# Kernel optimization log

Measured on AMD Instinct MI355X. Metric: run time of the kernel, lower is better.

The kernel has to match this reference:

```python
import jax, jax.numpy as jnp
import numpy as np

DIM = 1024
HEADS = 16
B, N = 4, 2048


def setup_inputs() -> dict:
    key = jax.random.key(0)
    ks = jax.random.split(key, 6)
    scale = DIM ** -0.5
    return {
        "x": jax.random.normal(ks[0], (B, N, DIM), dtype=jnp.float32),
        "mask": jax.random.randint(ks[1], (B, N, N), 0, 2) > 0,
        "Wqkv": jax.random.normal(ks[2], (DIM, 3 * DIM), dtype=jnp.float32) * scale,
        "bqkv": jax.random.normal(ks[3], (3 * DIM,), dtype=jnp.float32) * 0.02,
        "Wproj": jax.random.normal(ks[4], (DIM, DIM), dtype=jnp.float32) * scale,
        "bproj": jax.random.normal(ks[5], (DIM,), dtype=jnp.float32) * 0.02,
    }


def reference(x, mask, Wqkv, bqkv, Wproj, bproj):
    Bs, Ns, C = x.shape
    H = HEADS
    D = C // H
    scale = D ** -0.5
    qkv = x @ Wqkv + bqkv                       # [B, N, 3C]
    qkv = qkv.reshape(Bs, Ns, 3, H, D)          # split (three h d)
    q, k, v = jnp.moveaxis(qkv, 2, 0)           # each [B, N, H, D]
    q = q.transpose(0, 2, 1, 3)                 # [B, H, N, D]
    k = k.transpose(0, 2, 1, 3)
    v = v.transpose(0, 2, 1, 3)
    attn = jnp.einsum("bhnd,bhmd->bhnm", q, k) * scale  # [B, H, N, N]
    attn = jnp.where(mask[:, None, :, :], -jnp.inf, attn)
    attn = jax.nn.softmax(attn, axis=-1)
    out = jnp.einsum("bhnm,bhmd->bhnd", attn, v)        # [B, H, N, D]
    out = out.transpose(0, 2, 1, 3).reshape(Bs, Ns, C)  # [B, N, C]
    return out @ Wproj + bproj
```

## Files before the change

kernel.cpp:

```cpp
#include <hip/hip_runtime.h>
#include <cstdint>
#include <cstddef>

constexpr int kC = 1024;
constexpr int kH = 16;
constexpr int kB = 4;
constexpr int kN = 2048;
constexpr int kD = 64;

#define KQ_SCALE 0.18033688011112042f

typedef unsigned short u16;
typedef unsigned int   u32;
typedef unsigned long long u64;
typedef __bf16 v8bf  __attribute__((ext_vector_type(8)));
typedef __bf16 v4bf  __attribute__((ext_vector_type(4)));
typedef float  v4f   __attribute__((ext_vector_type(4)));
typedef u16    u16x8 __attribute__((ext_vector_type(8)));
typedef u16    u16x4 __attribute__((ext_vector_type(4)));
typedef u32    u32x4 __attribute__((ext_vector_type(4)));

__device__ inline u16 f2bf(float f) {
    union { float f; unsigned u; } v; v.f = f;
    unsigned r = v.u + 0x7FFFu + ((v.u >> 16) & 1u);
    return (u16)(r >> 16);
}

__device__ inline float fast_exp2(float x) {
#if __has_builtin(__builtin_amdgcn_exp2f)
    return __builtin_amdgcn_exp2f(x);
#else
    return __expf(x * 0.6931471805599453f);
#endif
}

__device__ inline void gl2lds16(const u16* g, u16* l) {
    __builtin_amdgcn_global_load_lds(
        (const __attribute__((address_space(1))) void*)g,
        (__attribute__((address_space(3))) void*)l, 16, 0, 0);
}

__global__ __launch_bounds__(256) void cast_bf16_kernel(
    const float* __restrict__ in, u16* __restrict__ outp)
{
    const int i = blockIdx.x * 256 + threadIdx.x;
    const float4 f = ((const float4*)in)[i];
    u16x4 o;
    o.x = f2bf(f.x); o.y = f2bf(f.y); o.z = f2bf(f.z); o.w = f2bf(f.w);
    ((u16x4*)outp)[i] = o;
}

__global__ __launch_bounds__(256) void tpose_cast_kernel(
    const float* __restrict__ W, u16* __restrict__ Wt, int R, int Cc)
{
    __shared__ u16 tile[64][65];
    const int c0 = blockIdx.x * 64;
    const int r0 = blockIdx.y * 64;
    const int t  = threadIdx.x;
#pragma unroll
    for (int it = 0; it < 16; ++it) {
        const int r = it * 4 + (t >> 6);
        const int c = t & 63;
        tile[c][r] = f2bf(W[(size_t)(r0 + r) * Cc + c0 + c]);
    }
    __syncthreads();
#pragma unroll
    for (int it = 0; it < 16; ++it) {
        const int rr = it * 4 + (t >> 6);
        const int cc = t & 63;
        Wt[(size_t)(c0 + rr) * R + r0 + cc] = tile[rr][cc];
    }
}

__global__ __launch_bounds__(256) void maskpack_kernel(
    const int* __restrict__ mask, u32* __restrict__ bits)
{
    const int lane = threadIdx.x & 63;
    const int wv   = threadIdx.x >> 6;
    const int nseg = kB * kN * 32;
    for (int seg = blockIdx.x * 4 + wv; seg < nseg; seg += gridDim.x * 4) {
        const size_t row = (size_t)(seg >> 5);
        const int s = seg & 31;
        const int m = mask[row * kN + s * 64 + lane];
        const u64 bal = __ballot(m != 0);
        if (lane == 0) ((u64*)bits)[row * 32 + s] = bal;
    }
}

template <int MODE>
__global__ __launch_bounds__(256, 4) void gemm_mfma_kernel(
    const u16* __restrict__ A, const u16* __restrict__ Bt,
    const float* __restrict__ bias, float* __restrict__ Cout,
    u16* __restrict__ qOut, u16* __restrict__ kOut, u16* __restrict__ vOut,
    int M, int N, int K)
{
    __shared__ u16 As0[128 * 32], Bs0[128 * 32];
    __shared__ u16 As1[128 * 32], Bs1[128 * 32];
    const int t    = threadIdx.x;
    const int w    = t >> 6;
    const int lane = t & 63;
    const int quad = lane >> 4;
    const int l16  = lane & 15;

    const int nby = M >> 7;
    const int q8  = (int)gridDim.x >> 3;
    const int bid = (int)blockIdx.x;
    const int swz = (bid & 7) * q8 + (bid >> 3);
    const int m0  = (swz % nby) * 128;
    const int n0  = (swz / nby) * 128;

    const int sr  = lane >> 2;
    const int scs = ((lane & 3) ^ ((sr >> 1) & 3)) * 8;
    const u16* Ag0 = A  + (size_t)(m0 + 32 * w      + sr) * K + scs;
    const u16* Ag1 = A  + (size_t)(m0 + 32 * w + 16 + sr) * K + scs;
    const u16* Bg0 = Bt + (size_t)(n0 + 32 * w      + sr) * K + scs;
    const u16* Bg1 = Bt + (size_t)(n0 + 32 * w + 16 + sr) * K + scs;

    v4f acc[4][4];
#pragma unroll
    for (int r = 0; r < 4; ++r)
#pragma unroll
        for (int c = 0; c < 4; ++c) acc[r][c] = (v4f){0.f, 0.f, 0.f, 0.f};

    const int mrow = (w >> 1) * 64;
    const int ncol = (w & 1) * 64;
    const int pch  = (quad ^ ((l16 >> 1) & 3)) * 8;

    auto stage = [&](u16* Asb, u16* Bsb, int k0) {
        gl2lds16(Ag0 + k0, Asb + (32 * w) * 32);
        gl2lds16(Ag1 + k0, Asb + (32 * w + 16) * 32);
        gl2lds16(Bg0 + k0, Bsb + (32 * w) * 32);
        gl2lds16(Bg1 + k0, Bsb + (32 * w + 16) * 32);
    };
    auto compute = [&](const u16* Asb, const u16* Bsb) {
        v8bf af[4], bfr[4];
#pragma unroll
        for (int r = 0; r < 4; ++r)
            af[r] = *(const v8bf*)(Asb + (mrow + r * 16 + l16) * 32 + pch);
#pragma unroll
        for (int c = 0; c < 4; ++c)
            bfr[c] = *(const v8bf*)(Bsb + (ncol + c * 16 + l16) * 32 + pch);
        __builtin_amdgcn_s_setprio(1);
#pragma unroll
        for (int r = 0; r < 4; ++r)
#pragma unroll
            for (int c = 0; c < 4; ++c)
                acc[r][c] = __builtin_amdgcn_mfma_f32_16x16x32_bf16(
                    af[r], bfr[c], acc[r][c], 0, 0, 0);
        __builtin_amdgcn_s_setprio(0);
    };

    u16 *ca = As0, *cb = Bs0, *na = As1, *nb_ = Bs1;
    stage(ca, cb, 0);

    for (int k0 = 0; k0 < K; k0 += 32) {
        const bool more = (k0 + 32 < K);
        if (more) stage(na, nb_, k0 + 32);
        if (more) {
            asm volatile("s_waitcnt vmcnt(4)" ::: "memory");
        } else {
            asm volatile("s_waitcnt vmcnt(0)" ::: "memory");
        }
        __builtin_amdgcn_s_barrier();
        __builtin_amdgcn_sched_barrier(0);
        compute(ca, cb);
        __builtin_amdgcn_s_barrier();
        u16* x1 = ca; ca = na; na = x1;
        u16* x2 = cb; cb = nb_; nb_ = x2;
    }

#pragma unroll
    for (int r = 0; r < 4; ++r) {
#pragma unroll
        for (int c = 0; c < 4; ++c) {
            const int col = n0 + ncol + c * 16 + l16;
            const float bv = bias[col];
#pragma unroll
            for (int reg = 0; reg < 4; ++reg) {
                const int row = m0 + mrow + r * 16 + quad * 4 + reg;
                float val = acc[r][c][reg] + bv;
                if (MODE == 0) {
                    Cout[(size_t)row * N + col] = val;
                } else {
                    const int which = col >> 10;
                    const int rem   = col & 1023;
                    const int h     = rem >> 6;
                    const int d     = rem & 63;
                    const int b     = row >> 11;
                    const int n     = row & 2047;
                    if (which == 0) val *= KQ_SCALE;
                    u16* dst = (which == 0) ? qOut : (which == 1) ? kOut : vOut;
                    dst[(((size_t)(b * kH + h)) * kN + n) * kD + d] = f2bf(val);
                }
            }
        }
    }
}

__global__ __launch_bounds__(256, 2) void attn_mfma_kernel(
    const u16* __restrict__ q, const u16* __restrict__ k,
    const u16* __restrict__ v, const u32* __restrict__ mbits,
    u16* __restrict__ out)
{
    __shared__ u16 Ks[2][128 * 64];
    __shared__ u16 Vt[2][64 * 128];

    const int t    = threadIdx.x;
    const int w    = t >> 6;
    const int lane = t & 63;
    const int quad = lane >> 4;
    const int l16  = lane & 15;

    const int bh    = blockIdx.x >> 4;
    const int tile0 = (blockIdx.x & 15) * 128;
    const int b     = bh >> 4;
    const int h     = bh & 15;

    const u16* qb = q + (size_t)bh * kN * kD;
    const u16* kb = k + (size_t)bh * kN * kD;
    const u16* vb = v + (size_t)bh * kN * kD;

    const int qrow0 = tile0 + w * 32 + l16;
    const int qrow1 = qrow0 + 16;
    v8bf qf[2][2];
    qf[0][0] = *(const v8bf*)(qb + (size_t)qrow0 * kD + quad * 8);
    qf[0][1] = *(const v8bf*)(qb + (size_t)qrow0 * kD + 32 + quad * 8);
    qf[1][0] = *(const v8bf*)(qb + (size_t)qrow1 * kD + quad * 8);
    qf[1][1] = *(const v8bf*)(qb + (size_t)qrow1 * kD + 32 + quad * 8);

    const int skr  = t >> 1;
    const int skh  = t & 1;
    const int vg   = t >> 4;
    const int vdq  = t & 15;
    const int vrow0 = (vg >> 2) * 32 + (vg & 3) * 4;

    const u16* kp = kb + (size_t)skr * kD + skh * 32;
    const u16* vp = vb + (size_t)vrow0 * kD + vdq * 4;
    const uint4* mp0 = (const uint4*)(mbits + ((size_t)b * kN + qrow0) * 64);
    const uint4* mp1 = (const uint4*)(mbits + ((size_t)b * kN + qrow1) * 64);

    u16x8 kpre[4];
    u16x4 vpre[8];
    uint4 mpre0, mpre1;
    auto issue_prefetch = [&]() {
#pragma unroll
        for (int i = 0; i < 4; ++i)
            kpre[i] = *(const u16x8*)(kp + i * 8);
#pragma unroll
        for (int i = 0; i < 8; ++i)
            vpre[i] = *(const u16x4*)(vp + (i < 4 ? i * 64 : 1024 + (i - 4) * 64));
        mpre0 = *mp0; mpre1 = *mp1;
        kp += 128 * kD; vp += 128 * kD; ++mp0; ++mp1;
    };

    v8bf onesf;
#pragma unroll
    for (int j = 0; j < 8; ++j) onesf[j] = (__bf16)1.0f;

    v4f oacc[2][4];
    v4f rsacc[2];
#pragma unroll
    for (int qs = 0; qs < 2; ++qs) {
        rsacc[qs] = (v4f){0.f, 0.f, 0.f, 0.f};
#pragma unroll
        for (int i = 0; i < 4; ++i) oacc[qs][i] = (v4f){0.f, 0.f, 0.f, 0.f};
    }

    issue_prefetch();

    for (int kt = 0; kt < kN / 128; ++kt) {
        u16* KsB = Ks[kt & 1];
        u16* VtB = Vt[kt & 1];

        {
            const int cb = skh * 4;
            u16* drow = &KsB[skr * 64];
#pragma unroll
            for (int i = 0; i < 4; ++i)
                *(u16x8*)(&drow[((cb + i) ^ (skr & 7)) * 8]) = kpre[i];
        }
        {
#pragma unroll
            for (int dd = 0; dd < 4; ++dd) {
                const int d = vdq * 4 + dd;
                u16x8 col;
#pragma unroll
                for (int j = 0; j < 8; ++j) col[j] = vpre[j][dd];
                *(u16x8*)(&VtB[d * 128 + ((vg ^ (d & 15)) * 8)]) = col;
            }
        }
        const uint4 mc0 = mpre0, mc1 = mpre1;
        if (kt + 1 < kN / 128) issue_prefetch();

        __syncthreads();

        const u32 mwa[2][4] = {{mc0.x, mc0.y, mc0.z, mc0.w},
                               {mc1.x, mc1.y, mc1.z, mc1.w}};
        v8bf pa[2][4];

#pragma unroll
        for (int nb = 0; nb < 8; ++nb) {
            const int krow = nb * 16 + l16;
            const v8bf kf0 = *(const v8bf*)(&KsB[krow * 64 + ((quad       ^ (krow & 7)) * 8)]);
            const v8bf kf1 = *(const v8bf*)(&KsB[krow * 64 + (((quad + 4) ^ (krow & 7)) * 8)]);
#pragma unroll
            for (int qs = 0; qs < 2; ++qs) {
                v4f s = (v4f){0.f, 0.f, 0.f, 0.f};
                s = __builtin_amdgcn_mfma_f32_16x16x32_bf16(kf0, qf[qs][0], s, 0, 0, 0);
                s = __builtin_amdgcn_mfma_f32_16x16x32_bf16(kf1, qf[qs][1], s, 0, 0, 0);

                const u32 m4 = (mwa[qs][nb >> 1] >> ((nb & 1) * 16 + quad * 4)) & 0xFu;
                float e0 = fast_exp2(s[0]);
                float e1 = fast_exp2(s[1]);
                float e2 = fast_exp2(s[2]);
                float e3 = fast_exp2(s[3]);
                e0 = (m4 & 1u) ? 0.f : e0;
                e1 = (m4 & 2u) ? 0.f : e1;
                e2 = (m4 & 4u) ? 0.f : e2;
                e3 = (m4 & 8u) ? 0.f : e3;

                pa[qs][nb >> 1][(nb & 1) * 4 + 0] = (__bf16)e0;
                pa[qs][nb >> 1][(nb & 1) * 4 + 1] = (__bf16)e1;
                pa[qs][nb >> 1][(nb & 1) * 4 + 2] = (__bf16)e2;
                pa[qs][nb >> 1][(nb & 1) * 4 + 3] = (__bf16)e3;
            }
        }

        __builtin_amdgcn_s_setprio(1);
#pragma unroll
        for (int qs = 0; qs < 2; ++qs)
#pragma unroll
            for (int ks = 0; ks < 4; ++ks)
                rsacc[qs] = __builtin_amdgcn_mfma_f32_16x16x32_bf16(
                    pa[qs][ks], onesf, rsacc[qs], 0, 0, 0);
#pragma unroll
        for (int ks = 0; ks < 4; ++ks)
#pragma unroll
            for (int db = 0; db < 4; ++db) {
                const int d = db * 16 + l16;
                const v8bf vf = *(const v8bf*)(&VtB[d * 128 + (((ks * 4 + quad) ^ (d & 15)) * 8)]);
#pragma unroll
                for (int qs = 0; qs < 2; ++qs)
                    oacc[qs][db] = __builtin_amdgcn_mfma_f32_16x16x32_bf16(
                        pa[qs][ks], vf, oacc[qs][db], 0, 0, 0);
            }
        __builtin_amdgcn_s_setprio(0);
    }

#pragma unroll
    for (int qs = 0; qs < 2; ++qs) {
        float inv[4];
#pragma unroll
        for (int reg = 0; reg < 4; ++reg) inv[reg] = 1.f / rsacc[qs][reg];
#pragma unroll
        for (int db = 0; db < 4; ++db)
#pragma unroll
            for (int reg = 0; reg < 4; ++reg) {
                const int row = tile0 + w * 32 + qs * 16 + quad * 4 + reg;
                const int col = h * 64 + db * 16 + l16;
                out[((size_t)(b * kN + row)) * kC + col] = f2bf(oacc[qs][db][reg] * inv[reg]);
            }
    }
}

extern "C" void kernel_launch(void* const* d_in, const int* in_sizes, int n_in,
                              void* d_out, int out_size, void* d_ws, size_t ws_size,
                              hipStream_t stream)
{
    const float* x     = (const float*)d_in[0];
    const int*   mask  = (const int*)d_in[1];
    const float* Wqkv  = (const float*)d_in[2];
    const float* bqkv  = (const float*)d_in[3];
    const float* Wproj = (const float*)d_in[4];
    const float* bproj = (const float*)d_in[5];
    float* out = (float*)d_out;

    const size_t nx = (size_t)kB * kN * kC;
    const size_t qkv_elems = (size_t)kB * kH * kN * kD;
    u16* xb     = (u16*)d_ws;
    u16* qbuf   = xb + nx;
    u16* kbuf   = qbuf + qkv_elems;
    u16* vbuf   = kbuf + qkv_elems;
    u16* aob    = vbuf + qkv_elems;
    u16* Wqkvt  = aob + nx;
    u16* Wprojt = Wqkvt + (size_t)3 * kC * kC;
    u32* mbits  = (u32*)(Wprojt + (size_t)kC * kC);

    maskpack_kernel<<<dim3(2048), dim3(256), 0, stream>>>(mask, mbits);
    cast_bf16_kernel<<<dim3(nx / 1024), dim3(256), 0, stream>>>(x, xb);
    tpose_cast_kernel<<<dim3(3 * kC / 64, kC / 64), dim3(256), 0, stream>>>(
        Wqkv, Wqkvt, kC, 3 * kC);
    tpose_cast_kernel<<<dim3(kC / 64, kC / 64), dim3(256), 0, stream>>>(
        Wproj, Wprojt, kC, kC);

    gemm_mfma_kernel<1><<<dim3((3 * kC / 128) * (kB * kN / 128)), dim3(256), 0, stream>>>(
        xb, Wqkvt, bqkv, nullptr, qbuf, kbuf, vbuf, kB * kN, 3 * kC, kC);

    attn_mfma_kernel<<<dim3(kB * kH * (kN / 128)), dim3(256), 0, stream>>>(
        qbuf, kbuf, vbuf, mbits, aob);

    gemm_mfma_kernel<0><<<dim3((kC / 128) * (kB * kN / 128)), dim3(256), 0, stream>>>(
        aob, Wprojt, bproj, out, nullptr, nullptr, nullptr, kB * kN, kC, kC);
}
```

Baseline: 368.4 us.

## Retile projection GEMMs to 256x256 blocks with 512 threads and BK=64

Replaces the 128x128, 256-thread GEMM with a 256x256 tile computed by 8 waves, each owning a 128x64 sub-tile. The K step grows to 64 with an XOR-swizzled LDS layout. Staging of the next A and B tiles is split across the MFMA phases to overlap global-to-LDS loads with compute. This raises data reuse per tile, but it cuts the block count sharply (128 blocks for the output projection, 384 for QKV) and uses a much larger LDS footprint, which may hurt occupancy and CU utilization.

```diff
diff --git a/kernel.cpp b/kernel.cpp
--- a/kernel.cpp
+++ b/kernel.cpp
@@ -14,11 +14,9 @@
 typedef unsigned int   u32;
 typedef unsigned long long u64;
 typedef __bf16 v8bf  __attribute__((ext_vector_type(8)));
-typedef __bf16 v4bf  __attribute__((ext_vector_type(4)));
 typedef float  v4f   __attribute__((ext_vector_type(4)));
 typedef u16    u16x8 __attribute__((ext_vector_type(8)));
 typedef u16    u16x4 __attribute__((ext_vector_type(4)));
-typedef u32    u32x4 __attribute__((ext_vector_type(4)));
 
 __device__ inline u16 f2bf(float f) {
     union { float f; unsigned u; } v; v.f = f;
@@ -88,97 +86,126 @@
 }
 
 template <int MODE>
-__global__ __launch_bounds__(256, 4) void gemm_mfma_kernel(
+__global__ __launch_bounds__(512, 2) void gemm256_kernel(
     const u16* __restrict__ A, const u16* __restrict__ Bt,
     const float* __restrict__ bias, float* __restrict__ Cout,
     u16* __restrict__ qOut, u16* __restrict__ kOut, u16* __restrict__ vOut,
     int M, int N, int K)
 {
-    __shared__ u16 As0[128 * 32], Bs0[128 * 32];
-    __shared__ u16 As1[128 * 32], Bs1[128 * 32];
+    __shared__ u16 lds[2][2][16384];
+
     const int t    = threadIdx.x;
     const int w    = t >> 6;
     const int lane = t & 63;
     const int quad = lane >> 4;
     const int l16  = lane & 15;
-
-    const int nby = M >> 7;
+    const int wm   = w >> 2;
+    const int wn   = w & 3;
+
+    const int nbm = M >> 8;
     const int q8  = (int)gridDim.x >> 3;
     const int bid = (int)blockIdx.x;
     const int swz = (bid & 7) * q8 + (bid >> 3);
-    const int m0  = (swz % nby) * 128;
-    const int n0  = (swz / nby) * 128;
-
-    const int sr  = lane >> 2;
-    const int scs = ((lane & 3) ^ ((sr >> 1) & 3)) * 8;
-    const u16* Ag0 = A  + (size_t)(m0 + 32 * w      + sr) * K + scs;
-    const u16* Ag1 = A  + (size_t)(m0 + 32 * w + 16 + sr) * K + scs;
-    const u16* Bg0 = Bt + (size_t)(n0 + 32 * w      + sr) * K + scs;
-    const u16* Bg1 = Bt + (size_t)(n0 + 32 * w + 16 + sr) * K + scs;
-
-    v4f acc[4][4];
-#pragma unroll
-    for (int r = 0; r < 4; ++r)
-#pragma unroll
-        for (int c = 0; c < 4; ++c) acc[r][c] = (v4f){0.f, 0.f, 0.f, 0.f};
-
-    const int mrow = (w >> 1) * 64;
-    const int ncol = (w & 1) * 64;
-    const int pch  = (quad ^ ((l16 >> 1) & 3)) * 8;
-
-    auto stage = [&](u16* Asb, u16* Bsb, int k0) {
-        gl2lds16(Ag0 + k0, Asb + (32 * w) * 32);
-        gl2lds16(Ag1 + k0, Asb + (32 * w + 16) * 32);
-        gl2lds16(Bg0 + k0, Bsb + (32 * w) * 32);
-        gl2lds16(Bg1 + k0, Bsb + (32 * w + 16) * 32);
+    const int m0  = (swz % nbm) * 256;
+    const int n0  = (swz / nbm) * 256;
+
+    const size_t halfStep = (size_t)128 * K;
+    const int s0 = t, s1 = 512 + t;
+    const int r0 = s0 >> 3, r1 = s1 >> 3;
+    const int c0 = ((s0 & 7) ^ (r0 & 7)) * 8;
+    const int c1 = ((s1 & 7) ^ (r1 & 7)) * 8;
+    const u16* gA0 = A  + (size_t)(m0 + r0) * K + c0;
+    const u16* gA1 = A  + (size_t)(m0 + r1) * K + c1;
+    const u16* gB0 = Bt + (size_t)(n0 + r0) * K + c0;
+    const u16* gB1 = Bt + (size_t)(n0 + r1) * K + c1;
+
+    v4f acc[8][4];
+#pragma unroll
+    for (int mi = 0; mi < 8; ++mi)
+#pragma unroll
+        for (int ni = 0; ni < 4; ++ni) acc[mi][ni] = (v4f){0.f, 0.f, 0.f, 0.f};
+
+    const int aRowB = (wm * 128 + l16) * 64;
+    const int bRowB = (wn * 64  + l16) * 64;
+    const int ch0   = ((quad    ) ^ (l16 & 7)) * 8;
+    const int ch1   = ((quad + 4) ^ (l16 & 7)) * 8;
+
+    auto stageA = [&](int buf, int kt) {
+        const int ko = kt * 64;
+        gl2lds16(gA0 + ko,            &lds[buf][0][       w * 512]);
+        gl2lds16(gA1 + ko,            &lds[buf][0][4096 + w * 512]);
+        gl2lds16(gA0 + halfStep + ko, &lds[buf][0][8192        + w * 512]);
+        gl2lds16(gA1 + halfStep + ko, &lds[buf][0][8192 + 4096 + w * 512]);
     };
-    auto compute = [&](const u16* Asb, const u16* Bsb) {
-        v8bf af[4], bfr[4];
-#pragma unroll
-        for (int r = 0; r < 4; ++r)
-            af[r] = *(const v8bf*)(Asb + (mrow + r * 16 + l16) * 32 + pch);
-#pragma unroll
-        for (int c = 0; c < 4; ++c)
-            bfr[c] = *(const v8bf*)(Bsb + (ncol + c * 16 + l16) * 32 + pch);
-        __builtin_amdgcn_s_setprio(1);
-#pragma unroll
-        for (int r = 0; r < 4; ++r)
-#pragma unroll
-            for (int c = 0; c < 4; ++c)
-                acc[r][c] = __builtin_amdgcn_mfma_f32_16x16x32_bf16(
-                    af[r], bfr[c], acc[r][c], 0, 0, 0);
-        __builtin_amdgcn_s_setprio(0);
+    auto stageB = [&](int buf, int kt) {
+        const int ko = kt * 64;
+        gl2lds16(gB0 + ko,            &lds[buf][1][       w * 512]);
+        gl2lds16(gB1 + ko,            &lds[buf][1][4096 + w * 512]);
+        gl2lds16(gB0 + halfStep + ko, &lds[buf][1][8192        + w * 512]);
+        gl2lds16(gB1 + halfStep + ko, &lds[buf][1][8192 + 4096 + w * 512]);
     };
 
-    u16 *ca = As0, *cb = Bs0, *na = As1, *nb_ = Bs1;
-    stage(ca, cb, 0);
-
-    for (int k0 = 0; k0 < K; k0 += 32) {
-        const bool more = (k0 + 32 < K);
-        if (more) stage(na, nb_, k0 + 32);
-        if (more) {
-            asm volatile("s_waitcnt vmcnt(4)" ::: "memory");
-        } else {
-            asm volatile("s_waitcnt vmcnt(0)" ::: "memory");
+    const int NT = K >> 6;
+    stageA(0, 0);
+    stageB(0, 0);
+
+    for (int kt = 0; kt < NT; ++kt) {
+        const int  cur  = kt & 1;
+        const int  nxt  = cur ^ 1;
+        const bool more = (kt + 1 < NT);
+        v8bf bfr[4][2];
+
+#pragma unroll
+        for (int p = 0; p < 4; ++p) {
+            if (p == 0) {
+                if (more) stageA(nxt, kt + 1);
+                if (more) asm volatile("s_waitcnt vmcnt(4)" ::: "memory");
+                else      asm volatile("s_waitcnt vmcnt(0)" ::: "memory");
+                __builtin_amdgcn_s_barrier();
+                __builtin_amdgcn_sched_barrier(0);
+#pragma unroll
+                for (int ni = 0; ni < 4; ++ni) {
+                    bfr[ni][0] = *(const v8bf*)(&lds[cur][1][bRowB + ni * 1024 + ch0]);
+                    bfr[ni][1] = *(const v8bf*)(&lds[cur][1][bRowB + ni * 1024 + ch1]);
+                }
+            }
+            v8bf a0[2], a1[2];
+#pragma unroll
+            for (int i = 0; i < 2; ++i) {
+                a0[i] = *(const v8bf*)(&lds[cur][0][aRowB + (2 * p + i) * 1024 + ch0]);
+                a1[i] = *(const v8bf*)(&lds[cur][0][aRowB + (2 * p + i) * 1024 + ch1]);
+            }
+            if (p == 1 && more) stageB(nxt, kt + 1);
+            if (p != 0) {
+                __builtin_amdgcn_s_barrier();
+                __builtin_amdgcn_sched_barrier(0);
+            }
+            __builtin_amdgcn_s_setprio(1);
+#pragma unroll
+            for (int i = 0; i < 2; ++i)
+#pragma unroll
+                for (int ni = 0; ni < 4; ++ni) {
+                    acc[2 * p + i][ni] = __builtin_amdgcn_mfma_f32_16x16x32_bf16(
+                        a0[i], bfr[ni][0], acc[2 * p + i][ni], 0, 0, 0);
+                    acc[2 * p + i][ni] = __builtin_amdgcn_mfma_f32_16x16x32_bf16(
+                        a1[i], bfr[ni][1], acc[2 * p + i][ni], 0, 0, 0);
+                }
+            __builtin_amdgcn_s_setprio(0);
+            __builtin_amdgcn_s_barrier();
+            __builtin_amdgcn_sched_barrier(0);
         }
-        __builtin_amdgcn_s_barrier();
-        __builtin_amdgcn_sched_barrier(0);
-        compute(ca, cb);
-        __builtin_amdgcn_s_barrier();
-        u16* x1 = ca; ca = na; na = x1;
-        u16* x2 = cb; cb = nb_; nb_ = x2;
-    }
-
-#pragma unroll
-    for (int r = 0; r < 4; ++r) {
-#pragma unroll
-        for (int c = 0; c < 4; ++c) {
-            const int col = n0 + ncol + c * 16 + l16;
-            const float bv = bias[col];
+    }
+
+#pragma unroll
+    for (int ni = 0; ni < 4; ++ni) {
+        const int col = n0 + wn * 64 + ni * 16 + l16;
+        const float bv = bias[col];
+#pragma unroll
+        for (int mi = 0; mi < 8; ++mi) {
 #pragma unroll
             for (int reg = 0; reg < 4; ++reg) {
-                const int row = m0 + mrow + r * 16 + quad * 4 + reg;
-                float val = acc[r][c][reg] + bv;
+                const int row = m0 + wm * 128 + mi * 16 + quad * 4 + reg;
+                float val = acc[mi][ni][reg] + bv;
                 if (MODE == 0) {
                     Cout[(size_t)row * N + col] = val;
                 } else {
@@ -393,12 +420,12 @@
     tpose_cast_kernel<<<dim3(kC / 64, kC / 64), dim3(256), 0, stream>>>(
         Wproj, Wprojt, kC, kC);
 
-    gemm_mfma_kernel<1><<<dim3((3 * kC / 128) * (kB * kN / 128)), dim3(256), 0, stream>>>(
+    gemm256_kernel<1><<<dim3((3 * kC / 256) * (kB * kN / 256)), dim3(512), 0, stream>>>(
         xb, Wqkvt, bqkv, nullptr, qbuf, kbuf, vbuf, kB * kN, 3 * kC, kC);
 
     attn_mfma_kernel<<<dim3(kB * kH * (kN / 128)), dim3(256), 0, stream>>>(
         qbuf, kbuf, vbuf, mbits, aob);
 
-    gemm_mfma_kernel<0><<<dim3((kC / 128) * (kB * kN / 128)), dim3(256), 0, stream>>>(
+    gemm256_kernel<0><<<dim3((kC / 256) * (kB * kN / 256)), dim3(512), 0, stream>>>(
         aob, Wprojt, bproj, out, nullptr, nullptr, nullptr, kB * kN, kC, kC);
 }
```

Measured after the change: 380.6 us. 3.3% more time.
